# Kernel optimization log

Hardware: AMD Instinct MI355X
Metric: run time of the kernel (lower is better)

Reference implementation:

```python
import jax, jax.numpy as jnp
import numpy as np

IN_FEATURES = 4096
OUT_FEATURES = 4096
SHARED_ROWS = 256
BATCH = 8192


def setup_inputs() -> dict:
    key = jax.random.key(0)
    k_x, k_w, k_b = jax.random.split(key, 3)
    x = jax.random.normal(k_x, (BATCH, IN_FEATURES), dtype=jnp.float32)
    shared_weights = jax.random.normal(k_w, (SHARED_ROWS, IN_FEATURES), dtype=jnp.float32)
    bias = jax.random.normal(k_b, (OUT_FEATURES,), dtype=jnp.float32)
    return {"x": x, "shared_weights": shared_weights, "bias": bias}


def reference(x, shared_weights, bias):
    # Faithful to torch: weight_matrix = shared_weights.repeat(out//shared, 1)
    reps = OUT_FEATURES // SHARED_ROWS
    weight_matrix = jnp.tile(shared_weights, (reps, 1))  # [out_features, in_features]
    # y = x @ W^T + b  -> [batch, out_features]
    return jnp.matmul(x, weight_matrix.T) + bias
```

## Files before the change

kernel.cpp:

```cpp
#include <hip/hip_runtime.h>
#include <cstdint>
#include <cstddef>

#define M_DIM 8192
#define N_DIM 256
#define K_DIM 4096
#define OUT_F 4096
#define BM 32
#define BN 128
#define BK 64
#define NTH 512
#define NKT (K_DIM / BK)

typedef float    float4_ __attribute__((ext_vector_type(4)));
typedef _Float16 half8   __attribute__((ext_vector_type(8)));
typedef _Float16 half4   __attribute__((ext_vector_type(4)));

__global__ __launch_bounds__(256) void convert_w_kernel(const float* __restrict__ w,
                                                        _Float16* __restrict__ wh) {
  int i = (blockIdx.x * 256 + threadIdx.x) * 8;
  float4_ f0 = *(const float4_*)(w + i);
  float4_ f1 = *(const float4_*)(w + i + 4);
  half8 h;
  h[0] = (_Float16)f0[0]; h[1] = (_Float16)f0[1];
  h[2] = (_Float16)f0[2]; h[3] = (_Float16)f0[3];
  h[4] = (_Float16)f1[0]; h[5] = (_Float16)f1[1];
  h[6] = (_Float16)f1[2]; h[7] = (_Float16)f1[3];
  *(half8*)(wh + i) = h;
}

__device__ __forceinline__ void load_bfrag(half8 b[2], const _Float16* __restrict__ wg,
                                           int kk) {
  b[0] = *(const half8*)(wg + kk);
  b[1] = *(const half8*)(wg + kk + 32);
}

__device__ __forceinline__ void stage_a(_Float16* __restrict__ As, int arow, int asw,
                                        float4_ a) {
  half4 h;
  h[0] = (_Float16)a[0]; h[1] = (_Float16)a[1];
  h[2] = (_Float16)a[2]; h[3] = (_Float16)a[3];
  *(half4*)(As + arow * BK + asw) = h;
}

__device__ __forceinline__ void mfma_step(float4_ acc[2], const half8 b[2],
                                          const _Float16* __restrict__ As,
                                          int l16, int quad) {
  __builtin_amdgcn_s_setprio(1);
#pragma unroll
  for (int ks = 0; ks < 2; ++ks) {
    const int off = ((ks * 4 + quad) ^ (l16 & 7)) << 3;
    half8 a0 = *(const half8*)(As + l16 * BK + off);
    half8 a1 = *(const half8*)(As + (16 + l16) * BK + off);
    acc[0] = __builtin_amdgcn_mfma_f32_16x16x32_f16(a0, b[ks], acc[0], 0, 0, 0);
    acc[1] = __builtin_amdgcn_mfma_f32_16x16x32_f16(a1, b[ks], acc[1], 0, 0, 0);
  }
  __builtin_amdgcn_s_setprio(0);
}

#define PHASE_BARRIER() do {                              \
    __builtin_amdgcn_sched_barrier(0);                    \
    asm volatile("s_waitcnt lgkmcnt(0)" ::: "memory");    \
    __builtin_amdgcn_s_barrier();                         \
    __builtin_amdgcn_sched_barrier(0);                    \
  } while (0)

__global__ __launch_bounds__(NTH, 4) void fused_kernel(const float* __restrict__ x,
                                                       const _Float16* __restrict__ wh,
                                                       const float* __restrict__ bias,
                                                       float* __restrict__ out) {
  __shared__ __align__(16) _Float16 As[2][BM * BK];
  __shared__ __align__(16) float Ssh[BM][BN + 4];
  __shared__ __align__(16) float bsh[16 * BN];

  const int tid  = threadIdx.x;
  const int wv   = tid >> 6;
  const int lane = tid & 63;
  const int quad = lane >> 4;
  const int l16  = lane & 15;
  const int m0   = blockIdx.x * BM;
  const int nb   = blockIdx.y * BN;

  {
    const float4_* b4 = (const float4_*)bias;
    float4_* bs4 = (float4_*)bsh;
    int rep = tid >> 5, c4 = tid & 31;
    bs4[tid] = b4[rep * (N_DIM / 4) + (nb >> 2) + c4];
  }

  const int arow = tid >> 4;
  const int ac4  = tid & 15;
  const int asw  = ((((ac4 >> 1) ^ (arow & 7)) << 3) | ((ac4 & 1) << 2));
  const float* xg = x + (size_t)(m0 + arow) * K_DIM + ac4 * 4;

  const _Float16* wg = wh + (size_t)(nb + wv * 16 + l16) * K_DIM + quad * 8;

  float4_ acc[2];
  acc[0] = (float4_){0.f, 0.f, 0.f, 0.f};
  acc[1] = (float4_){0.f, 0.f, 0.f, 0.f};

  half8 bA[2], bB[2];
  float4_ aP0 = __builtin_nontemporal_load((const float4_*)(xg));
  float4_ aP1 = __builtin_nontemporal_load((const float4_*)(xg + BK));
  load_bfrag(bA, wg, 0);
  stage_a(As[0], arow, asw, aP0);
  aP0 = __builtin_nontemporal_load((const float4_*)(xg + 2 * BK));
  PHASE_BARRIER();

  for (int kt = 0; kt < NKT; kt += 2) {
    load_bfrag(bB, wg, (kt + 1) * BK);
    stage_a(As[1], arow, asw, aP1);
    if (kt + 3 < NKT)
      aP1 = __builtin_nontemporal_load((const float4_*)(xg + (kt + 3) * BK));
    mfma_step(acc, bA, As[0], l16, quad);
    PHASE_BARRIER();

    if (kt + 2 < NKT) {
      load_bfrag(bA, wg, (kt + 2) * BK);
      stage_a(As[0], arow, asw, aP0);
      if (kt + 4 < NKT)
        aP0 = __builtin_nontemporal_load((const float4_*)(xg + (kt + 4) * BK));
    }
    mfma_step(acc, bB, As[1], l16, quad);
    PHASE_BARRIER();
  }

#pragma unroll
  for (int mf = 0; mf < 2; ++mf)
#pragma unroll
    for (int r = 0; r < 4; ++r)
      Ssh[mf * 16 + quad * 4 + r][wv * 16 + l16] = acc[mf][r];
  PHASE_BARRIER();

  float4_* out4 = (float4_*)out;
  const float4_* bs4 = (const float4_*)bsh;
#pragma unroll
  for (int p = 0; p < 2; ++p) {
    const int row = wv * 4 + p * 2 + (lane >> 5);
    const int c4  = lane & 31;
    float4_ sv = *(const float4_*)(&Ssh[row][c4 * 4]);
    const size_t obase = (size_t)(m0 + row) * (OUT_F / 4) + (nb >> 2);
#pragma unroll
    for (int rep = 0; rep < 16; ++rep)
      __builtin_nontemporal_store(sv + bs4[rep * (BN / 4) + c4],
                                  out4 + obase + rep * (N_DIM / 4) + c4);
  }
}

extern "C" void kernel_launch(void* const* d_in, const int* in_sizes, int n_in,
                              void* d_out, int out_size, void* d_ws, size_t ws_size,
                              hipStream_t stream) {
  const float* x    = (const float*)d_in[0];
  const float* w    = (const float*)d_in[1];
  const float* bias = (const float*)d_in[2];
  float* out        = (float*)d_out;
  _Float16* wh      = (_Float16*)d_ws;

  convert_w_kernel<<<(N_DIM * K_DIM) / (256 * 8), 256, 0, stream>>>(w, wh);
  fused_kernel<<<dim3(M_DIM / BM, 2), NTH, 0, stream>>>(x, wh, bias, out);
}
```

Before: 282.8 us.

## Split fused GEMM-expand into separate GEMM and broadcast-expand kernels

The fused kernel, which both computed the 256-column product and wrote the 16x-replicated output with bias, becomes two kernels. The GEMM kernel now writes the small product P (8192x256) to workspace. A new expand kernel reads P and writes full contiguous output rows with bias, so each row is stored as one long contiguous span. This decouples the write-heavy expansion from the compute kernel and gives better-coalesced stores, at the cost of an extra launch and an 8 MB round trip through P.

Measured after the change: 287.0 us. About the same (+1.5%).

```diff
diff --git a/kernel.cpp b/kernel.cpp
--- a/kernel.cpp
+++ b/kernel.cpp
@@ -65,13 +65,11 @@
     __builtin_amdgcn_sched_barrier(0);                    \
   } while (0)
 
-__global__ __launch_bounds__(NTH, 4) void fused_kernel(const float* __restrict__ x,
-                                                       const _Float16* __restrict__ wh,
-                                                       const float* __restrict__ bias,
-                                                       float* __restrict__ out) {
+__global__ __launch_bounds__(NTH, 4) void gemm_p_kernel(const float* __restrict__ x,
+                                                        const _Float16* __restrict__ wh,
+                                                        float* __restrict__ P) {
   __shared__ __align__(16) _Float16 As[2][BM * BK];
   __shared__ __align__(16) float Ssh[BM][BN + 4];
-  __shared__ __align__(16) float bsh[16 * BN];
 
   const int tid  = threadIdx.x;
   const int wv   = tid >> 6;
@@ -80,13 +78,6 @@
   const int l16  = lane & 15;
   const int m0   = blockIdx.x * BM;
   const int nb   = blockIdx.y * BN;
-
-  {
-    const float4_* b4 = (const float4_*)bias;
-    float4_* bs4 = (float4_*)bsh;
-    int rep = tid >> 5, c4 = tid & 31;
-    bs4[tid] = b4[rep * (N_DIM / 4) + (nb >> 2) + c4];
-  }
 
   const int arow = tid >> 4;
   const int ac4  = tid & 15;
@@ -132,18 +123,39 @@
       Ssh[mf * 16 + quad * 4 + r][wv * 16 + l16] = acc[mf][r];
   PHASE_BARRIER();
 
-  float4_* out4 = (float4_*)out;
-  const float4_* bs4 = (const float4_*)bsh;
+  float4_* P4 = (float4_*)P;
 #pragma unroll
   for (int p = 0; p < 2; ++p) {
     const int row = wv * 4 + p * 2 + (lane >> 5);
     const int c4  = lane & 31;
     float4_ sv = *(const float4_*)(&Ssh[row][c4 * 4]);
-    const size_t obase = (size_t)(m0 + row) * (OUT_F / 4) + (nb >> 2);
+    P4[(size_t)(m0 + row) * (N_DIM / 4) + (nb >> 2) + c4] = sv;
+  }
+}
+
+__global__ __launch_bounds__(256) void expand_kernel(const float* __restrict__ P,
+                                                     const float* __restrict__ bias,
+                                                     float* __restrict__ out) {
+  __shared__ __align__(16) float bsh[OUT_F];
+  const int tid = threadIdx.x;
+  const float4_* b4 = (const float4_*)bias;
+  float4_* bs4 = (float4_*)bsh;
 #pragma unroll
-    for (int rep = 0; rep < 16; ++rep)
-      __builtin_nontemporal_store(sv + bs4[rep * (BN / 4) + c4],
-                                  out4 + obase + rep * (N_DIM / 4) + c4);
+  for (int p = 0; p < 4; ++p) bs4[p * 256 + tid] = b4[p * 256 + tid];
+  __syncthreads();
+
+  const int ml  = tid >> 6;
+  const int c64 = tid & 63;
+  const float4_* P4 = (const float4_*)P;
+
+#pragma unroll
+  for (int pass = 0; pass < 2; ++pass) {
+    const int m = blockIdx.x * 8 + pass * 4 + ml;
+    float4_ s = P4[(size_t)m * (N_DIM / 4) + c64];
+    float4_* orow = (float4_*)(out + (size_t)m * OUT_F);
+#pragma unroll
+    for (int c = 0; c < 16; ++c)
+      __builtin_nontemporal_store(s + bs4[c * 64 + c64], orow + c * 64 + c64);
   }
 }
 
@@ -155,7 +167,9 @@
   const float* bias = (const float*)d_in[2];
   float* out        = (float*)d_out;
   _Float16* wh      = (_Float16*)d_ws;
+  float* P          = (float*)((char*)d_ws + (4u << 20));
 
   convert_w_kernel<<<(N_DIM * K_DIM) / (256 * 8), 256, 0, stream>>>(w, wh);
-  fused_kernel<<<dim3(M_DIM / BM, 2), NTH, 0, stream>>>(x, wh, bias, out);
+  gemm_p_kernel<<<dim3(M_DIM / BM, 2), NTH, 0, stream>>>(x, wh, P);
+  expand_kernel<<<M_DIM / 8, 256, 0, stream>>>(P, bias, out);
 }
```
